# Performance work log

Measured on AMD Instinct MI355X. Metric: run time of the kernel, lower is better.

## Reference

```python
import jax, jax.numpy as jnp
import numpy as np

N = 50000      # nodes
E = 600000     # edges
A = 8          # max attrs per node
DT = 64        # node type embed dim
DA = 64        # node attr embed dim
C = DT + DA    # annotation dim = GGNN channels
T = 16         # num node types
TE = 4         # num edge types
L = 4          # num_agg_steps
B = 256        # num graphs
VATTR = 1000   # num node attrs
ENC = 128      # encoder_output_dim
NCLS = 10      # decoder output classes


def setup_inputs() -> dict:
    key = jax.random.key(0)
    ks = jax.random.split(key, 16)
    s = 0.05
    x_type = jax.random.randint(ks[0], (N,), 0, T)
    x_attrs = jax.random.randint(ks[1], (N, A), 0, VATTR)
    x_attrs_mask = jax.random.randint(ks[2], (N,), 1, A + 1)  # >=1 valid attr per node
    edge_index = jax.random.randint(ks[3], (2, E), 0, N)
    edge_attr = jax.random.randint(ks[4], (E,), 0, TE)
    batch = jnp.sort(jax.random.randint(ks[5], (N,), 0, B))
    return {
        'x_type': x_type, 'x_attrs': x_attrs, 'x_attrs_mask': x_attrs_mask,
        'edge_index': edge_index, 'edge_attr': edge_attr,
        'num_graphs': int(B), 'batch': batch,
        'type_emb': jax.random.normal(ks[6], (T, DT)) * s,
        'attr_emb': jax.random.normal(ks[7], (VATTR, DA)) * s,
        'W_msg': jax.random.normal(ks[8], (L, TE, C, C)) * s,
        'W_ih': jax.random.normal(ks[9], (3 * C, C)) * s,
        'W_hh': jax.random.normal(ks[10], (3 * C, C)) * s,
        'b_ih': jnp.zeros((3 * C,)),
        'b_hh': jnp.zeros((3 * C,)),
        'w_attn': jax.random.normal(ks[11], (C,)) * s,
        'b_attn': jnp.zeros(()),
        'W_enc': jax.random.normal(ks[12], (T * C, ENC)) * s,
        'b_enc': jnp.zeros((ENC,)),
        'W_dec': jax.random.normal(ks[13], (ENC, NCLS)) * s,
        'b_dec': jnp.zeros((NCLS,)),
    }


def _gru_cell(m, h, W_ih, W_hh, b_ih, b_hh):
    gi = m @ W_ih.T + b_ih            # [N, 3C]
    gh = h @ W_hh.T + b_hh            # [N, 3C]
    ir, iz, inn = jnp.split(gi, 3, axis=-1)
    hr, hz, hn = jnp.split(gh, 3, axis=-1)
    r = jax.nn.sigmoid(ir + hr)
    z = jax.nn.sigmoid(iz + hz)
    n = jnp.tanh(inn + r * hn)
    return (1.0 - z) * n + z * h


def reference(x_type, x_attrs, x_attrs_mask, edge_index, edge_attr, num_graphs, batch,
              type_emb, attr_emb, W_msg, W_ih, W_hh, b_ih, b_hh,
              w_attn, b_attn, W_enc, b_enc, W_dec, b_dec):
    n = x_type.shape[0]
    # --- embed node types and ragged-mean attribute embeddings ---
    t_emb = type_emb[x_type]                                   # [N, DT]
    a_all = attr_emb[x_attrs]                                  # [N, A, DA]
    valid = (jnp.arange(A)[None, :] < x_attrs_mask[:, None]).astype(a_all.dtype)
    a_emb = (a_all * valid[..., None]).sum(1) / jnp.maximum(x_attrs_mask, 1)[:, None].astype(a_all.dtype)
    x = jnp.concatenate([t_emb, a_emb], axis=1)                # [N, C]

    # --- GatedGraphConv with per-edge-type weights (sum aggregation + GRU) ---
    src, dst = edge_index[0], edge_index[1]
    for l in range(L):
        h_all = jnp.einsum('nc,tcd->tnd', x, W_msg[l])         # [TE, N, C]
        m_e = h_all.reshape(TE * n, C)[edge_attr * n + src]    # [E, C] gather per edge
        m = jax.ops.segment_sum(m_e, dst, num_segments=n)      # [N, C]
        x = _gru_cell(m, x, W_ih, W_hh, b_ih, b_hh)

    # --- per-(graph, node_type) segment mean (zeros for empty groups) ---
    seg = batch * T + x_type                                   # [N]
    S = num_graphs * T
    sums = jax.ops.segment_sum(x, seg, num_segments=S)         # [B*T, C]
    cnt = jax.ops.segment_sum(jnp.ones((n,), x.dtype), seg, num_segments=S)
    agg = jnp.where(cnt[:, None] > 0, sums / jnp.maximum(cnt, 1.0)[:, None], 0.0)
    agg = agg.reshape(num_graphs, T, C)                        # [B, T, C]

    # --- attention over node types, flatten, encode, decode ---
    w = agg @ w_attn + b_attn                                  # [B, T]
    attn = jax.nn.softmax(w, axis=-1)
    flat = (attn[..., None] * agg).reshape(num_graphs, T * C)  # [B, T*C]
    enc = flat @ W_enc + b_enc                                 # [B, ENC]
    return enc @ W_dec + b_dec                                 # [B, NCLS]
```

## Files before the change

### kernel.cpp

```cpp
#include <hip/hip_runtime.h>
#include <hip/hip_bf16.h>

#define NN 50000
#define EE 600000
#define AA 8
#define CC 128
#define TT 16
#define TE 4
#define LL 4
#define BB 256
#define ENC 128
#define NCLS 10

typedef __attribute__((ext_vector_type(8))) short bf16x8;
typedef __attribute__((ext_vector_type(4))) float fx4;
typedef __attribute__((ext_vector_type(4))) uint ux4;

__device__ __forceinline__ float b2f(ushort u) {
    union { float f; uint32_t i; } v; v.i = ((uint32_t)u) << 16; return v.f;
}
__device__ __forceinline__ ushort f2b(float f) {
    union { float f; uint32_t i; } v; v.f = f;
    uint32_t x = v.i;
    x += 0x7FFFu + ((x >> 16) & 1u);
    return (ushort)(x >> 16);
}
__device__ __forceinline__ float ldw(const void* p, long i, int isf) {
    return isf ? ((const float*)p)[i] : b2f(((const ushort*)p)[i]);
}
__device__ __forceinline__ float sigm(float t) { return 1.f / (1.f + __expf(-t)); }

__global__ void sniff_kernel(int* flag, const void* W_enc_raw) {
    const ushort* u = (const ushort*)W_enc_raw;
    int good = 0;
    for (int i = 0; i < 256; ++i) {
        ushort v = u[i];
        int ex = (v >> 7) & 0xFF;
        if (v == 0 || (ex >= 100 && ex <= 126)) ++good;
    }
    *flag = (good >= 230) ? 0 : 1;
}

__global__ __launch_bounds__(256) void wmsgT_kernel(ushort* __restrict__ wT,
                                                    const void* __restrict__ W,
                                                    const int* __restrict__ flag) {
    const int isf = *flag;
    int idx = blockIdx.x * 256 + threadIdx.x;
    int lt = idx >> 14, rem = idx & 16383, d = rem >> 7, c = rem & 127;
    long src = ((long)lt << 14) + c * 128 + d;
    wT[idx] = isf ? f2b(((const float*)W)[src]) : ((const ushort*)W)[src];
}

__global__ __launch_bounds__(256) void wgru_kernel(ushort* __restrict__ wgb,
                                                   const void* __restrict__ Wih,
                                                   const void* __restrict__ Whh,
                                                   const int* __restrict__ flag) {
    const int isf = *flag;
    int idx = blockIdx.x * 256 + threadIdx.x;
    if (idx >= 98304) return;
    int ih = (idx < 49152);
    int off = ih ? idx : idx - 49152;
    wgb[idx] = f2b(ldw(ih ? Wih : Whh, off, isf));
}

__global__ __launch_bounds__(256) void wencT_kernel(ushort* __restrict__ wencT,
                                                    const void* __restrict__ W_enc,
                                                    const int* __restrict__ flag) {
    const int isf = *flag;
    int idx = blockIdx.x * 256 + threadIdx.x;
    int j = idx >> 11, k = idx & 2047;
    wencT[idx] = f2b(ldw(W_enc, (long)k * ENC + j, isf));
}

__global__ __launch_bounds__(256) void bconv_kernel(float* __restrict__ cvt,
                                                    const void* __restrict__ bih, const void* __restrict__ bhh,
                                                    const void* __restrict__ b_enc, const void* __restrict__ w_attn,
                                                    const void* __restrict__ b_dec, const void* __restrict__ b_attn,
                                                    const void* __restrict__ W_dec,
                                                    const int* __restrict__ flag) {
    const int isf = *flag;
    int i = blockIdx.x * 256 + threadIdx.x;
    if (i < 384) cvt[i] = ldw(bih, i, isf);
    else if (i < 768) cvt[i] = ldw(bhh, i - 384, isf);
    else if (i < 896) cvt[i] = ldw(b_enc, i - 768, isf);
    else if (i < 1024) cvt[i] = ldw(w_attn, i - 896, isf);
    else if (i < 1034) cvt[i] = ldw(b_dec, i - 1024, isf);
    else if (i == 1034) cvt[i] = ldw(b_attn, 0, isf);
    else if (i >= 1040 && i < 2320) cvt[i] = ldw(W_dec, i - 1040, isf);
}

__global__ __launch_bounds__(256) void embed_kernel(
    ushort* __restrict__ xbf,
    const int* __restrict__ x_type, const int* __restrict__ x_attrs,
    const int* __restrict__ x_mask, const void* __restrict__ type_emb,
    const void* __restrict__ attr_emb, const int* __restrict__ flag) {
    const int isf = *flag;
    int idx = blockIdx.x * 256 + threadIdx.x;
    int n = idx >> 6, c = idx & 63;
    if (n >= NN) return;
    int ty = x_type[n];
    xbf[n * CC + c] = f2b(ldw(type_emb, ty * 64 + c, isf));
    int cnt = x_mask[n];
    float s = 0.f;
    for (int a = 0; a < cnt; ++a) s += ldw(attr_emb, x_attrs[n * AA + a] * 64 + c, isf);
    xbf[n * CC + 64 + c] = f2b(s / (float)cnt);
}

__global__ __launch_bounds__(256) void deg_kernel(int* __restrict__ cnt, const int* __restrict__ ei) {
    int e = blockIdx.x * 256 + threadIdx.x;
    if (e < EE) atomicAdd(&cnt[ei[EE + e]], 1);
}
__global__ __launch_bounds__(256) void scan1_kernel(int* __restrict__ cnt, int* __restrict__ btot) {
    __shared__ int s[256];
    int tid = threadIdx.x, i = blockIdx.x * 256 + tid;
    int v = (i < NN) ? cnt[i] : 0;
    s[tid] = v; __syncthreads();
    for (int off = 1; off < 256; off <<= 1) {
        int t = (tid >= off) ? s[tid - off] : 0; __syncthreads();
        s[tid] += t; __syncthreads();
    }
    if (i < NN) cnt[i] = s[tid] - v;
    if (tid == 255) btot[blockIdx.x] = s[255];
}
__global__ __launch_bounds__(256) void scan2_kernel(int* __restrict__ btot, int nb) {
    __shared__ int s[256];
    int tid = threadIdx.x;
    int v = (tid < nb) ? btot[tid] : 0;
    s[tid] = v; __syncthreads();
    for (int off = 1; off < 256; off <<= 1) {
        int t = (tid >= off) ? s[tid - off] : 0; __syncthreads();
        s[tid] += t; __syncthreads();
    }
    if (tid < nb) btot[tid] = s[tid] - v;
}
__global__ __launch_bounds__(256) void scan3_kernel(int* __restrict__ cnt, const int* __restrict__ btot) {
    int i = blockIdx.x * 256 + threadIdx.x;
    if (i < NN) cnt[i] += btot[blockIdx.x];
}
__global__ __launch_bounds__(256) void fill_kernel(uint* __restrict__ csr, int* __restrict__ cnt,
                                                   const int* __restrict__ ei, const int* __restrict__ ea) {
    int e = blockIdx.x * 256 + threadIdx.x;
    if (e >= EE) return;
    int d = ei[EE + e];
    int pos = atomicAdd(&cnt[d], 1);
    csr[pos] = (uint)ei[e] | ((uint)ea[e] << 16);
}

__global__ __launch_bounds__(256) void msg_mfma4(
    ushort* __restrict__ h4, const ushort* __restrict__ xbf, const ushort* __restrict__ wT) {
    __shared__ ushort h_s[4][32][128];
    int tid = threadIdx.x;
    int t = tid >> 6, l = tid & 63;
    int node0 = blockIdx.x * 32;
    int lr = l & 15, lk = (l >> 4) * 8;
    bf16x8 af[2][4];
#pragma unroll
    for (int rt = 0; rt < 2; ++rt)
#pragma unroll
        for (int ks = 0; ks < 4; ++ks)
            af[rt][ks] = *(const bf16x8*)&xbf[(size_t)(node0 + rt * 16 + lr) * CC + ks * 32 + lk];
#pragma unroll
    for (int ct = 0; ct < 8; ++ct) {
        bf16x8 bfr[4];
#pragma unroll
        for (int ks = 0; ks < 4; ++ks)
            bfr[ks] = *(const bf16x8*)&wT[(size_t)(t * 128 + ct * 16 + lr) * 128 + ks * 32 + lk];
        fx4 acc0 = {0.f, 0.f, 0.f, 0.f}, acc1 = {0.f, 0.f, 0.f, 0.f};
#pragma unroll
        for (int ks = 0; ks < 4; ++ks) {
            acc0 = __builtin_amdgcn_mfma_f32_16x16x32_bf16(af[0][ks], bfr[ks], acc0, 0, 0, 0);
            acc1 = __builtin_amdgcn_mfma_f32_16x16x32_bf16(af[1][ks], bfr[ks], acc1, 0, 0, 0);
        }
#pragma unroll
        for (int r = 0; r < 4; ++r) {
            int nl = (l >> 4) * 4 + r;
            h_s[t][nl][ct * 16 + lr]      = f2b(acc0[r]);
            h_s[t][nl + 16][ct * 16 + lr] = f2b(acc1[r]);
        }
    }
    __syncthreads();
    const uint* ls = (const uint*)&h_s[0][0][0];
#pragma unroll
    for (int q = 0; q < 8; ++q) {
        int i4 = q * 256 + tid;
        int t2 = i4 >> 9, rem = i4 & 511;
        int node = rem >> 4, chunk = rem & 15;
        if (node0 + node < NN) {
            ux4 v = *(const ux4*)&ls[i4 * 4];
            *(ux4*)&h4[((size_t)t2 * NN + node0 + node) * CC + chunk * 8] = v;
        }
    }
}

__global__ __launch_bounds__(256) void gather_kernel(
    ushort* __restrict__ mbf, const ushort* __restrict__ h4,
    const uint* __restrict__ csr, const int* __restrict__ endp) {
    int w = threadIdx.x >> 6, l = threadIdx.x & 63;
    int node = blockIdx.x * 4 + w;
    int start = (node == 0) ? 0 : endp[node - 1];
    int end = endp[node];
    int c0 = l * 2;
    float s0 = 0.f, s1 = 0.f;
    for (int i = start; i < end; ++i) {
        uint pk = csr[i];
        uint src = pk & 0xFFFFu, t = pk >> 16;
        uint hv = *(const uint*)&h4[(((size_t)t * NN + src) << 7) + c0];
        s0 += b2f((ushort)(hv & 0xFFFFu));
        s1 += b2f((ushort)(hv >> 16));
    }
    *(uint*)&mbf[((size_t)node << 7) + c0] = (uint)f2b(s0) | ((uint)f2b(s1) << 16);
}

template <int AGG>
__global__ __launch_bounds__(256) void gru_mfma(
    ushort* __restrict__ xbf, const ushort* __restrict__ mbf,
    const ushort* __restrict__ wgb, const float* __restrict__ cvt,
    float* __restrict__ sums, float* __restrict__ cnta,
    const int* __restrict__ batch, const int* __restrict__ x_type) {
    int tid = threadIdx.x;
    int w = tid >> 6, l = tid & 63;
    int node0 = blockIdx.x * 32;
    int lr = l & 15, lk = (l >> 4) * 8;
    bf16x8 mf[2][4], xf[2][4];
#pragma unroll
    for (int rt = 0; rt < 2; ++rt)
#pragma unroll
        for (int ks = 0; ks < 4; ++ks) {
            size_t ro = (size_t)(node0 + rt * 16 + lr) * CC + ks * 32 + lk;
            mf[rt][ks] = *(const bf16x8*)&mbf[ro];
            xf[rt][ks] = *(const bf16x8*)&xbf[ro];
        }
    __syncthreads();
#pragma unroll
    for (int cc = 0; cc < 2; ++cc) {
        int ct = w * 2 + cc;
        int row0 = ct * 16 + lr;
        fx4 ai[3][2], ah[3][2];
#pragma unroll
        for (int s = 0; s < 3; ++s)
#pragma unroll
            for (int rt = 0; rt < 2; ++rt) { ai[s][rt] = (fx4){0,0,0,0}; ah[s][rt] = (fx4){0,0,0,0}; }
#pragma unroll
        for (int ks = 0; ks < 4; ++ks) {
            int ko = ks * 32 + lk;
            bf16x8 bI[3], bH[3];
#pragma unroll
            for (int s = 0; s < 3; ++s) {
                bI[s] = *(const bf16x8*)&wgb[(size_t)(s * 128 + row0) * 128 + ko];
                bH[s] = *(const bf16x8*)&wgb[49152 + (size_t)(s * 128 + row0) * 128 + ko];
            }
#pragma unroll
            for (int s = 0; s < 3; ++s)
#pragma unroll
                for (int rt = 0; rt < 2; ++rt) {
                    ai[s][rt] = __builtin_amdgcn_mfma_f32_16x16x32_bf16(mf[rt][ks], bI[s], ai[s][rt], 0, 0, 0);
                    ah[s][rt] = __builtin_amdgcn_mfma_f32_16x16x32_bf16(xf[rt][ks], bH[s], ah[s][rt], 0, 0, 0);
                }
        }
        float bi0 = cvt[row0],        bh0 = cvt[384 + row0];
        float bi1 = cvt[128 + row0],  bh1 = cvt[512 + row0];
        float bi2 = cvt[256 + row0],  bh2 = cvt[640 + row0];
#pragma unroll
        for (int rt = 0; rt < 2; ++rt)
#pragma unroll
            for (int r = 0; r < 4; ++r) {
                int node = node0 + rt * 16 + (l >> 4) * 4 + r;
                if (node >= NN) continue;
                float rg = sigm(ai[0][rt][r] + bi0 + ah[0][rt][r] + bh0);
                float zg = sigm(ai[1][rt][r] + bi1 + ah[1][rt][r] + bh1);
                float ny = ai[2][rt][r] + bi2 + rg * (ah[2][rt][r] + bh2);
                float ng = 2.f * sigm(2.f * ny) - 1.f;
                size_t xi = (size_t)node * CC + row0;
                float xo = b2f(xbf[xi]);
                float xn = (1.f - zg) * ng + zg * xo;
                xbf[xi] = f2b(xn);
                if (AGG) {
                    int seg = batch[node] * TT + x_type[node];
                    atomicAdd(&sums[(size_t)seg * CC + row0], xn);
                    if (row0 == 0) atomicAdd(&cnta[seg], 1.0f);
                }
            }
    }
}

__global__ __launch_bounds__(256) void attnflat_kernel(
    ushort* __restrict__ flatbf, const float* __restrict__ sums, const float* __restrict__ cnt,
    const float* __restrict__ cvt) {
    __shared__ float agg_s[TT][CC + 1];
    __shared__ float wpart[TT][8];
    __shared__ float attn_s[TT];
    int b = blockIdx.x, tid = threadIdx.x;
#pragma unroll
    for (int q = 0; q < 8; ++q) {
        int idx = tid + q * 256;
        int t = idx >> 7, c = idx & 127;
        float cv = cnt[b * TT + t];
        agg_s[t][c] = cv > 0.f ? sums[(size_t)(b * TT + t) * CC + c] / cv : 0.f;
    }
    __syncthreads();
    if (tid < 128) {
        int t = tid >> 3, p = tid & 7;
        float acc = 0.f;
        for (int i = 0; i < 16; ++i) acc += agg_s[t][p * 16 + i] * cvt[896 + p * 16 + i];
        wpart[t][p] = acc;
    }
    __syncthreads();
    if (tid < 16) {
        float acc = cvt[1034];
        for (int p = 0; p < 8; ++p) acc += wpart[tid][p];
        attn_s[tid] = acc;
    }
    __syncthreads();
    if (tid == 0) {
        float mx = attn_s[0];
        for (int t = 1; t < TT; ++t) mx = fmaxf(mx, attn_s[t]);
        float ssum = 0.f, ex[TT];
        for (int t = 0; t < TT; ++t) { ex[t] = __expf(attn_s[t] - mx); ssum += ex[t]; }
        for (int t = 0; t < TT; ++t) attn_s[t] = ex[t] / ssum;
    }
    __syncthreads();
#pragma unroll
    for (int q = 0; q < 8; ++q) {
        int idx = tid + q * 256;
        int t = idx >> 7, c = idx & 127;
        flatbf[(size_t)b * 2048 + idx] = f2b(agg_s[t][c] * attn_s[t]);
    }
}

__global__ __launch_bounds__(256) void enc_mfma(
    float* __restrict__ encp, const ushort* __restrict__ flatbf, const ushort* __restrict__ wencT) {
    int tid = threadIdx.x;
    int w = tid >> 6, l = tid & 63;
    int bid = blockIdx.x;
    int m0 = (bid >> 2) * 16;
    int kc = (bid & 3) * 512;
    int lr = l & 15, lk = (l >> 4) * 8;
    fx4 acc0 = {0,0,0,0}, acc1 = {0,0,0,0};
    int ct0 = w * 2, ct1 = w * 2 + 1;
#pragma unroll
    for (int ks = 0; ks < 16; ++ks) {
        int ko = kc + ks * 32 + lk;
        bf16x8 af = *(const bf16x8*)&flatbf[(size_t)(m0 + lr) * 2048 + ko];
        bf16x8 b0 = *(const bf16x8*)&wencT[(size_t)(ct0 * 16 + lr) * 2048 + ko];
        bf16x8 b1 = *(const bf16x8*)&wencT[(size_t)(ct1 * 16 + lr) * 2048 + ko];
        acc0 = __builtin_amdgcn_mfma_f32_16x16x32_bf16(af, b0, acc0, 0, 0, 0);
        acc1 = __builtin_amdgcn_mfma_f32_16x16x32_bf16(af, b1, acc1, 0, 0, 0);
    }
#pragma unroll
    for (int r = 0; r < 4; ++r) {
        int row = m0 + (l >> 4) * 4 + r;
        encp[(size_t)(bid & 3) * BB * ENC + (size_t)row * ENC + ct0 * 16 + lr] = acc0[r];
        encp[(size_t)(bid & 3) * BB * ENC + (size_t)row * ENC + ct1 * 16 + lr] = acc1[r];
    }
}

__global__ __launch_bounds__(256) void dec_kernel(
    void* __restrict__ out, const float* __restrict__ encp, const float* __restrict__ cvt,
    const int* __restrict__ flag) {
    const int isf = *flag;
    __shared__ float encs[ENC];
    int b = blockIdx.x, tid = threadIdx.x;
    if (tid < 128) {
        float e = cvt[768 + tid];
#pragma unroll
        for (int p = 0; p < 4; ++p) e += encp[(size_t)p * BB * ENC + (size_t)b * ENC + tid];
        encs[tid] = e;
    }
    __syncthreads();
    if (tid < NCLS) {
        float acc = cvt[1024 + tid];
        for (int j = 0; j < ENC; ++j) acc += encs[j] * cvt[1040 + j * NCLS + tid];
        int oi = b * NCLS + tid;
        if (isf) ((float*)out)[oi] = acc;
        else ((ushort*)out)[oi] = f2b(acc);
    }
}

extern "C" void kernel_launch(void* const* d_in, const int* in_sizes, int n_in,
                              void* d_out, int out_size, void* d_ws, size_t ws_size,
                              hipStream_t stream) {
    const int* x_type      = (const int*)d_in[0];
    const int* x_attrs     = (const int*)d_in[1];
    const int* x_mask      = (const int*)d_in[2];
    const int* edge_index  = (const int*)d_in[3];
    const int* edge_attr   = (const int*)d_in[4];
    const int* batch       = (const int*)d_in[6];
    const void* type_emb   = d_in[7];
    const void* attr_emb   = d_in[8];
    const void* W_msg      = d_in[9];
    const void* W_ih       = d_in[10];
    const void* W_hh       = d_in[11];
    const void* b_ih       = d_in[12];
    const void* b_hh       = d_in[13];
    const void* w_attn     = d_in[14];
    const void* b_attn     = d_in[15];
    const void* W_enc      = d_in[16];
    const void* b_enc      = d_in[17];
    const void* W_dec      = d_in[18];
    const void* b_dec      = d_in[19];

    char* p = (char*)d_ws;
    ushort* xbf   = (ushort*)p;          p += (size_t)NN * CC * 2;
    ushort* mbf   = (ushort*)p;          p += (size_t)NN * CC * 2;
    ushort* h4    = (ushort*)p;          p += (size_t)4 * NN * CC * 2;
    ushort* wT    = (ushort*)p;          p += (size_t)16 * 128 * 128 * 2;
    ushort* wgb   = (ushort*)p;          p += (size_t)2 * 384 * 128 * 2;
    ushort* wencT = (ushort*)p;          p += (size_t)ENC * 2048 * 2;
    ushort* flatbf= (ushort*)p;          p += (size_t)BB * 2048 * 2;
    float*  encp  = (float*)p;           p += (size_t)4 * BB * ENC * 4;
    float*  cvt   = (float*)p;           p += 2320 * 4;
    float*  sums  = (float*)p;           p += (size_t)BB * TT * CC * 4;
    float*  cnta  = (float*)p;           p += (size_t)BB * TT * 4;
    uint*   csr   = (uint*)p;            p += (size_t)EE * 4;
    int*    cptr  = (int*)p;             p += (size_t)NN * 4;
    int*    btot  = (int*)p;             p += 256 * 4;
    int*    flag  = (int*)p;

    sniff_kernel<<<1, 1, 0, stream>>>(flag, W_enc);
    wmsgT_kernel<<<1024, 256, 0, stream>>>(wT, W_msg, flag);
    wgru_kernel<<<384, 256, 0, stream>>>(wgb, W_ih, W_hh, flag);
    wencT_kernel<<<1024, 256, 0, stream>>>(wencT, W_enc, flag);
    bconv_kernel<<<10, 256, 0, stream>>>(cvt, b_ih, b_hh, b_enc, w_attn, b_dec, b_attn, W_dec, flag);
    embed_kernel<<<(NN * 64) / 256, 256, 0, stream>>>(xbf, x_type, x_attrs, x_mask,
                                                      type_emb, attr_emb, flag);

    const int NB = (NN + 255) / 256;
    hipMemsetAsync(cptr, 0, (size_t)NN * sizeof(int), stream);
    deg_kernel<<<(EE + 255) / 256, 256, 0, stream>>>(cptr, edge_index);
    scan1_kernel<<<NB, 256, 0, stream>>>(cptr, btot);
    scan2_kernel<<<1, 256, 0, stream>>>(btot, NB);
    scan3_kernel<<<NB, 256, 0, stream>>>(cptr, btot);
    fill_kernel<<<(EE + 255) / 256, 256, 0, stream>>>(csr, cptr, edge_index, edge_attr);

    hipMemsetAsync(sums, 0, (size_t)(BB * TT * CC + BB * TT) * sizeof(float), stream);

    const int tile_grid = (NN + 31) / 32;
    for (int l = 0; l < LL; ++l) {
        msg_mfma4<<<tile_grid, 256, 0, stream>>>(h4, xbf, wT + (size_t)l * 4 * 128 * 128);
        gather_kernel<<<NN / 4, 256, 0, stream>>>(mbf, h4, csr, cptr);
        if (l < LL - 1)
            gru_mfma<0><<<tile_grid, 256, 0, stream>>>(xbf, mbf, wgb, cvt, sums, cnta, batch, x_type);
        else
            gru_mfma<1><<<tile_grid, 256, 0, stream>>>(xbf, mbf, wgb, cvt, sums, cnta, batch, x_type);
    }

    attnflat_kernel<<<BB, 256, 0, stream>>>(flatbf, sums, cnta, cvt);
    enc_mfma<<<64, 256, 0, stream>>>(encp, flatbf, wencT);
    dec_kernel<<<BB, 256, 0, stream>>>(d_out, encp, cvt, flag);
}
```

Baseline: 797.7 us.

## Fuse message transform, edge gather and GRU into one per-layer kernel

Each layer now uses one kernel instead of three. It first gathers raw neighbor features into four per-edge-type sums in shared memory, then applies the four edge-type weight matrices to those sums with MFMA, then runs the GRU on the result. This reorders the algebra as sum-then-transform, which removes the 4xN×C h4 intermediate and the global m buffer and cuts launches. Ping-pong x buffers replace the in-place update. The costs are a per-node serialized gather inside the tile with branchy type dispatch, 16 MFMA-K steps per output tile, and changed rounding because the per-type sums are rounded to bf16 before the matmul.

```diff
diff --git a/kernel.cpp b/kernel.cpp
--- a/kernel.cpp
+++ b/kernel.cpp
@@ -11,10 +11,10 @@
 #define BB 256
 #define ENC 128
 #define NCLS 10
+#define SROW 136
 
 typedef __attribute__((ext_vector_type(8))) short bf16x8;
 typedef __attribute__((ext_vector_type(4))) float fx4;
-typedef __attribute__((ext_vector_type(4))) uint ux4;
 
 __device__ __forceinline__ float b2f(ushort u) {
     union { float f; uint32_t i; } v; v.i = ((uint32_t)u) << 16; return v.f;
@@ -146,91 +146,81 @@
     csr[pos] = (uint)ei[e] | ((uint)ea[e] << 16);
 }
 
-__global__ __launch_bounds__(256) void msg_mfma4(
-    ushort* __restrict__ h4, const ushort* __restrict__ xbf, const ushort* __restrict__ wT) {
-    __shared__ ushort h_s[4][32][128];
-    int tid = threadIdx.x;
-    int t = tid >> 6, l = tid & 63;
-    int node0 = blockIdx.x * 32;
-    int lr = l & 15, lk = (l >> 4) * 8;
-    bf16x8 af[2][4];
-#pragma unroll
-    for (int rt = 0; rt < 2; ++rt)
-#pragma unroll
-        for (int ks = 0; ks < 4; ++ks)
-            af[rt][ks] = *(const bf16x8*)&xbf[(size_t)(node0 + rt * 16 + lr) * CC + ks * 32 + lk];
-#pragma unroll
-    for (int ct = 0; ct < 8; ++ct) {
-        bf16x8 bfr[4];
-#pragma unroll
-        for (int ks = 0; ks < 4; ++ks)
-            bfr[ks] = *(const bf16x8*)&wT[(size_t)(t * 128 + ct * 16 + lr) * 128 + ks * 32 + lk];
-        fx4 acc0 = {0.f, 0.f, 0.f, 0.f}, acc1 = {0.f, 0.f, 0.f, 0.f};
-#pragma unroll
-        for (int ks = 0; ks < 4; ++ks) {
-            acc0 = __builtin_amdgcn_mfma_f32_16x16x32_bf16(af[0][ks], bfr[ks], acc0, 0, 0, 0);
-            acc1 = __builtin_amdgcn_mfma_f32_16x16x32_bf16(af[1][ks], bfr[ks], acc1, 0, 0, 0);
-        }
-#pragma unroll
-        for (int r = 0; r < 4; ++r) {
-            int nl = (l >> 4) * 4 + r;
-            h_s[t][nl][ct * 16 + lr]      = f2b(acc0[r]);
-            h_s[t][nl + 16][ct * 16 + lr] = f2b(acc1[r]);
-        }
-    }
-    __syncthreads();
-    const uint* ls = (const uint*)&h_s[0][0][0];
-#pragma unroll
-    for (int q = 0; q < 8; ++q) {
-        int i4 = q * 256 + tid;
-        int t2 = i4 >> 9, rem = i4 & 511;
-        int node = rem >> 4, chunk = rem & 15;
-        if (node0 + node < NN) {
-            ux4 v = *(const ux4*)&ls[i4 * 4];
-            *(ux4*)&h4[((size_t)t2 * NN + node0 + node) * CC + chunk * 8] = v;
-        }
-    }
-}
-
-__global__ __launch_bounds__(256) void gather_kernel(
-    ushort* __restrict__ mbf, const ushort* __restrict__ h4,
-    const uint* __restrict__ csr, const int* __restrict__ endp) {
-    int w = threadIdx.x >> 6, l = threadIdx.x & 63;
-    int node = blockIdx.x * 4 + w;
-    int start = (node == 0) ? 0 : endp[node - 1];
-    int end = endp[node];
-    int c0 = l * 2;
-    float s0 = 0.f, s1 = 0.f;
-    for (int i = start; i < end; ++i) {
-        uint pk = csr[i];
-        uint src = pk & 0xFFFFu, t = pk >> 16;
-        uint hv = *(const uint*)&h4[(((size_t)t * NN + src) << 7) + c0];
-        s0 += b2f((ushort)(hv & 0xFFFFu));
-        s1 += b2f((ushort)(hv >> 16));
-    }
-    *(uint*)&mbf[((size_t)node << 7) + c0] = (uint)f2b(s0) | ((uint)f2b(s1) << 16);
-}
-
 template <int AGG>
-__global__ __launch_bounds__(256) void gru_mfma(
-    ushort* __restrict__ xbf, const ushort* __restrict__ mbf,
-    const ushort* __restrict__ wgb, const float* __restrict__ cvt,
+__global__ __launch_bounds__(256) void layer_kernel(
+    const ushort* __restrict__ xin, ushort* __restrict__ xout,
+    const ushort* __restrict__ wT4, const ushort* __restrict__ wgb,
+    const float* __restrict__ cvt,
+    const uint* __restrict__ csr, const int* __restrict__ endp,
     float* __restrict__ sums, float* __restrict__ cnta,
     const int* __restrict__ batch, const int* __restrict__ x_type) {
+    __shared__ ushort s_bf[4][32][SROW];
+    __shared__ ushort m_bf[32][SROW];
     int tid = threadIdx.x;
     int w = tid >> 6, l = tid & 63;
     int node0 = blockIdx.x * 32;
-    int lr = l & 15, lk = (l >> 4) * 8;
+    int lr = l & 15, lk = (l >> 4) * 8, hi = l >> 4;
+
+    int c0 = l * 2;
+#pragma unroll 1
+    for (int q = 0; q < 8; ++q) {
+        int nloc = w * 8 + q;
+        int node = node0 + nloc;
+        int start = 0, end = 0;
+        if (node < NN) { start = (node == 0) ? 0 : endp[node - 1]; end = endp[node]; }
+        float t0a = 0.f, t0b = 0.f, t1a = 0.f, t1b = 0.f;
+        float t2a = 0.f, t2b = 0.f, t3a = 0.f, t3b = 0.f;
+        for (int i = start; i < end; ++i) {
+            uint pk = csr[i];
+            uint src = pk & 0xFFFFu, t = pk >> 16;
+            uint hv = *(const uint*)&xin[((size_t)src << 7) + c0];
+            float lo = b2f((ushort)(hv & 0xFFFFu)), hh = b2f((ushort)(hv >> 16));
+            if (t == 0)      { t0a += lo; t0b += hh; }
+            else if (t == 1) { t1a += lo; t1b += hh; }
+            else if (t == 2) { t2a += lo; t2b += hh; }
+            else             { t3a += lo; t3b += hh; }
+        }
+        *(uint*)&s_bf[0][nloc][c0] = (uint)f2b(t0a) | ((uint)f2b(t0b) << 16);
+        *(uint*)&s_bf[1][nloc][c0] = (uint)f2b(t1a) | ((uint)f2b(t1b) << 16);
+        *(uint*)&s_bf[2][nloc][c0] = (uint)f2b(t2a) | ((uint)f2b(t2b) << 16);
+        *(uint*)&s_bf[3][nloc][c0] = (uint)f2b(t3a) | ((uint)f2b(t3b) << 16);
+    }
+    __syncthreads();
+
+#pragma unroll
+    for (int rt = 0; rt < 2; ++rt) {
+        bf16x8 sf[4][4];
+#pragma unroll
+        for (int t = 0; t < 4; ++t)
+#pragma unroll
+            for (int ks = 0; ks < 4; ++ks)
+                sf[t][ks] = *(const bf16x8*)&s_bf[t][rt * 16 + lr][ks * 32 + lk];
+#pragma unroll
+        for (int cc = 0; cc < 2; ++cc) {
+            int ctg = w * 2 + cc;
+            fx4 acc = {0.f, 0.f, 0.f, 0.f};
+#pragma unroll
+            for (int t = 0; t < 4; ++t)
+#pragma unroll
+                for (int ks = 0; ks < 4; ++ks) {
+                    bf16x8 bf = *(const bf16x8*)&wT4[(size_t)(t * 128 + ctg * 16 + lr) * 128 + ks * 32 + lk];
+                    acc = __builtin_amdgcn_mfma_f32_16x16x32_bf16(sf[t][ks], bf, acc, 0, 0, 0);
+                }
+#pragma unroll
+            for (int r = 0; r < 4; ++r)
+                m_bf[rt * 16 + hi * 4 + r][ctg * 16 + lr] = f2b(acc[r]);
+        }
+    }
+    __syncthreads();
+
     bf16x8 mf[2][4], xf[2][4];
 #pragma unroll
     for (int rt = 0; rt < 2; ++rt)
 #pragma unroll
         for (int ks = 0; ks < 4; ++ks) {
-            size_t ro = (size_t)(node0 + rt * 16 + lr) * CC + ks * 32 + lk;
-            mf[rt][ks] = *(const bf16x8*)&mbf[ro];
-            xf[rt][ks] = *(const bf16x8*)&xbf[ro];
+            mf[rt][ks] = *(const bf16x8*)&m_bf[rt * 16 + lr][ks * 32 + lk];
+            xf[rt][ks] = *(const bf16x8*)&xin[(size_t)(node0 + rt * 16 + lr) * CC + ks * 32 + lk];
         }
-    __syncthreads();
 #pragma unroll
     for (int cc = 0; cc < 2; ++cc) {
         int ct = w * 2 + cc;
@@ -264,16 +254,16 @@
         for (int rt = 0; rt < 2; ++rt)
 #pragma unroll
             for (int r = 0; r < 4; ++r) {
-                int node = node0 + rt * 16 + (l >> 4) * 4 + r;
+                int node = node0 + rt * 16 + hi * 4 + r;
                 if (node >= NN) continue;
                 float rg = sigm(ai[0][rt][r] + bi0 + ah[0][rt][r] + bh0);
                 float zg = sigm(ai[1][rt][r] + bi1 + ah[1][rt][r] + bh1);
                 float ny = ai[2][rt][r] + bi2 + rg * (ah[2][rt][r] + bh2);
                 float ng = 2.f * sigm(2.f * ny) - 1.f;
                 size_t xi = (size_t)node * CC + row0;
-                float xo = b2f(xbf[xi]);
+                float xo = b2f(xin[xi]);
                 float xn = (1.f - zg) * ng + zg * xo;
-                xbf[xi] = f2b(xn);
+                xout[xi] = f2b(xn);
                 if (AGG) {
                     int seg = batch[node] * TT + x_type[node];
                     atomicAdd(&sums[(size_t)seg * CC + row0], xn);
@@ -400,9 +390,8 @@
     const void* b_dec      = d_in[19];
 
     char* p = (char*)d_ws;
-    ushort* xbf   = (ushort*)p;          p += (size_t)NN * CC * 2;
-    ushort* mbf   = (ushort*)p;          p += (size_t)NN * CC * 2;
-    ushort* h4    = (ushort*)p;          p += (size_t)4 * NN * CC * 2;
+    ushort* xbf0  = (ushort*)p;          p += (size_t)NN * CC * 2;
+    ushort* xbf1  = (ushort*)p;          p += (size_t)NN * CC * 2;
     ushort* wT    = (ushort*)p;          p += (size_t)16 * 128 * 128 * 2;
     ushort* wgb   = (ushort*)p;          p += (size_t)2 * 384 * 128 * 2;
     ushort* wencT = (ushort*)p;          p += (size_t)ENC * 2048 * 2;
@@ -421,7 +410,7 @@
     wgru_kernel<<<384, 256, 0, stream>>>(wgb, W_ih, W_hh, flag);
     wencT_kernel<<<1024, 256, 0, stream>>>(wencT, W_enc, flag);
     bconv_kernel<<<10, 256, 0, stream>>>(cvt, b_ih, b_hh, b_enc, w_attn, b_dec, b_attn, W_dec, flag);
-    embed_kernel<<<(NN * 64) / 256, 256, 0, stream>>>(xbf, x_type, x_attrs, x_mask,
+    embed_kernel<<<(NN * 64) / 256, 256, 0, stream>>>(xbf0, x_type, x_attrs, x_mask,
                                                       type_emb, attr_emb, flag);
 
     const int NB = (NN + 255) / 256;
@@ -436,12 +425,15 @@
 
     const int tile_grid = (NN + 31) / 32;
     for (int l = 0; l < LL; ++l) {
-        msg_mfma4<<<tile_grid, 256, 0, stream>>>(h4, xbf, wT + (size_t)l * 4 * 128 * 128);
-        gather_kernel<<<NN / 4, 256, 0, stream>>>(mbf, h4, csr, cptr);
+        const ushort* xin = (l & 1) ? xbf1 : xbf0;
+        ushort* xout      = (l & 1) ? xbf0 : xbf1;
+        const ushort* wT4 = wT + (size_t)l * 4 * 128 * 128;
         if (l < LL - 1)
-            gru_mfma<0><<<tile_grid, 256, 0, stream>>>(xbf, mbf, wgb, cvt, sums, cnta, batch, x_type);
+            layer_kernel<0><<<tile_grid, 256, 0, stream>>>(xin, xout, wT4, wgb, cvt,
+                                                           csr, cptr, sums, cnta, batch, x_type);
         else
-            gru_mfma<1><<<tile_grid, 256, 0, stream>>>(xbf, mbf, wgb, cvt, sums, cnta, batch, x_type);
+            layer_kernel<1><<<tile_grid, 256, 0, stream>>>(xin, xout, wT4, wgb, cvt,
+                                                           csr, cptr, sums, cnta, batch, x_type);
     }
 
     attnflat_kernel<<<BB, 256, 0, stream>>>(flatbf, sums, cnta, cvt);
```

Result: slower. 1.436 ms (+80.0%).
